# Performance work log

Hardware: AMD Instinct MI355X
Metric: run time of the kernel (lower is better)

## Reference

```python
import jax, jax.numpy as jnp
import numpy as np

N = 50000
E = 800000
F_IN = 96
HID = 128
NCLS = 40
EPS = 0.0  # GINConv default eps


def _mlp(h, W1, b1, W2, b2):
    # Linear -> ReLU -> Linear
    h = jax.nn.relu(h @ W1 + b1)
    return h @ W2 + b2


def _gin_conv(x, edge_index, W1, b1, W2, b2):
    src, dst = edge_index[0], edge_index[1]
    # sum-aggregate neighbor features: scatter-add x[src] into dst
    agg = jax.ops.segment_sum(x[src], dst, num_segments=N)
    return _mlp((1.0 + EPS) * x + agg, W1, b1, W2, b2)


def setup_inputs() -> dict:
    key = jax.random.key(0)
    ks = jax.random.split(key, 12)

    def lin(kw, fan_in, fan_out):
        bound = 1.0 / np.sqrt(fan_in)
        k1, k2 = jax.random.split(kw)
        W = jax.random.uniform(k1, (fan_in, fan_out), jnp.float32, -bound, bound)
        b = jax.random.uniform(k2, (fan_out,), jnp.float32, -bound, bound)
        return W, b

    x = jax.random.normal(ks[0], (N, F_IN), jnp.float32)
    edge_index = jax.random.randint(ks[1], (2, E), 0, N, jnp.int64)
    W1a, b1a = lin(ks[2], F_IN, HID)
    W2a, b2a = lin(ks[3], HID, HID)
    W1b, b1b = lin(ks[4], HID, HID)
    W2b, b2b = lin(ks[5], HID, HID)
    Wfc, bfc = lin(ks[6], HID, NCLS)
    return {"x": x, "edge_index": edge_index,
            "W1a": W1a, "b1a": b1a, "W2a": W2a, "b2a": b2a,
            "W1b": W1b, "b1b": b1b, "W2b": W2b, "b2b": b2b,
            "Wfc": Wfc, "bfc": bfc}


def reference(x, edge_index, W1a, b1a, W2a, b2a, W1b, b1b, W2b, b2b, Wfc, bfc):
    h = _gin_conv(x, edge_index, W1a, b1a, W2a, b2a)
    h = jax.nn.relu(h)
    h = _gin_conv(h, edge_index, W1b, b1b, W2b, b2b)
    return h @ Wfc + bfc  # [N, NCLS]
```

## Files before the change

### kernel.cpp

```cpp
#include <hip/hip_runtime.h>

constexpr int N_NODES = 50000;
constexpr int N_EDGES = 800000;
constexpr int F_INPUT = 96;
constexpr int HID = 128;
constexpr int NCLS = 40;
constexpr int CAP = 64;

typedef __attribute__((ext_vector_type(8))) short short8;
typedef __attribute__((ext_vector_type(4))) float f32x4;

__device__ __forceinline__ float bf2f(unsigned int u16) {
    unsigned int x = u16 << 16;
    return __builtin_bit_cast(float, x);
}
__device__ __forceinline__ unsigned short f2bf(float f) {
    unsigned int x = __builtin_bit_cast(unsigned int, f);
    x += 0x7fffu + ((x >> 16) & 1u);
    return (unsigned short)(x >> 16);
}

__global__ __launch_bounds__(256) void prep_all(
    const float* __restrict__ x,
    const float* __restrict__ W1a, const float* __restrict__ W2a,
    const float* __restrict__ W1b, const float* __restrict__ W2b,
    const float* __restrict__ b2b, const float* __restrict__ Wfc,
    const float* __restrict__ bfc, const int* __restrict__ ei,
    unsigned short* __restrict__ W1aT, unsigned short* __restrict__ W2aT,
    unsigned short* __restrict__ W1bT, unsigned short* __restrict__ WcT,
    float* __restrict__ bc, int* __restrict__ cnt,
    unsigned short* __restrict__ bucket, unsigned short* __restrict__ xb) {
    const int b = blockIdx.x;
    const int tid = threadIdx.x;
    if (b < 33) {
        int idx = b * 256 + tid;
        if (idx < 64 * 128) {
            int n = idx >> 7, k = idx & 127;
            float s = 0.f;
            if (n < NCLS) {
                for (int j = 0; j < 128; ++j) s += W2b[k * 128 + j] * Wfc[j * NCLS + n];
            }
            WcT[idx] = f2bf(s);
        } else if (idx < 64 * 128 + 64) {
            int n = idx - 64 * 128;
            float s = 0.f;
            if (n < NCLS) {
                s = bfc[n];
                for (int j = 0; j < 128; ++j) s += b2b[j] * Wfc[j * NCLS + n];
            }
            bc[n] = s;
        }
    } else if (b < 81) {
        int idx = (b - 33) * 256 + tid;
        int n = idx / 96, k = idx % 96;
        W1aT[idx] = f2bf(W1a[k * 128 + n]);
    } else if (b < 145) {
        int idx = (b - 81) * 256 + tid;
        int n = idx >> 7, k = idx & 127;
        W2aT[idx] = f2bf(W2a[k * 128 + n]);
    } else if (b < 209) {
        int idx = (b - 145) * 256 + tid;
        int n = idx >> 7, k = idx & 127;
        W1bT[idx] = f2bf(W1b[k * 128 + n]);
    } else if (b < 991) {
        int e4 = ((b - 209) * 256 + tid) * 4;
        if (e4 < N_EDGES) {
            int4 s = *reinterpret_cast<const int4*>(&ei[e4]);
            int4 d = *reinterpret_cast<const int4*>(&ei[N_EDGES + e4]);
            int p0 = atomicAdd(&cnt[d.x], 1);
            if (p0 < CAP) bucket[d.x * CAP + p0] = (unsigned short)s.x;
            int p1 = atomicAdd(&cnt[d.y], 1);
            if (p1 < CAP) bucket[d.y * CAP + p1] = (unsigned short)s.y;
            int p2 = atomicAdd(&cnt[d.z], 1);
            if (p2 < CAP) bucket[d.z * CAP + p2] = (unsigned short)s.z;
            int p3 = atomicAdd(&cnt[d.w], 1);
            if (p3 < CAP) bucket[d.w * CAP + p3] = (unsigned short)s.w;
        }
    } else {
        int e4 = ((b - 991) * 256 + tid) * 4;
        if (e4 < N_NODES * F_INPUT) {
            float4 v = *reinterpret_cast<const float4*>(&x[e4]);
            uint2 o;
            o.x = (unsigned int)f2bf(v.x) | ((unsigned int)f2bf(v.y) << 16);
            o.y = (unsigned int)f2bf(v.z) | ((unsigned int)f2bf(v.w) << 16);
            *reinterpret_cast<uint2*>(&xb[e4]) = o;
        }
    }
}

template<int F>
__global__ __launch_bounds__(256) void gather_bf(const unsigned short* __restrict__ X,
                                                 const int* __restrict__ cnt,
                                                 const unsigned short* __restrict__ bucket,
                                                 unsigned short* __restrict__ OUT) {
    const int wave = threadIdx.x >> 6;
    const int lane = threadIdx.x & 63;
    const int node = blockIdx.x * 4 + wave;
    if (node >= N_NODES) return;
    int deg = cnt[node];
    if (deg > CAP) deg = CAP;
    const unsigned short* idx = &bucket[node * CAP];
    const int f = lane * 2;
    const bool act = (f < F);
    float a0 = 0.f, a1 = 0.f;
    int j = 0;
    for (; j + 3 < deg; j += 4) {
        int s0 = idx[j], s1 = idx[j + 1], s2 = idx[j + 2], s3 = idx[j + 3];
        if (act) {
            unsigned int v0 = *reinterpret_cast<const unsigned int*>(&X[(size_t)s0 * F + f]);
            unsigned int v1 = *reinterpret_cast<const unsigned int*>(&X[(size_t)s1 * F + f]);
            unsigned int v2 = *reinterpret_cast<const unsigned int*>(&X[(size_t)s2 * F + f]);
            unsigned int v3 = *reinterpret_cast<const unsigned int*>(&X[(size_t)s3 * F + f]);
            a0 += bf2f(v0 & 0xffff) + bf2f(v1 & 0xffff) + bf2f(v2 & 0xffff) + bf2f(v3 & 0xffff);
            a1 += bf2f(v0 >> 16) + bf2f(v1 >> 16) + bf2f(v2 >> 16) + bf2f(v3 >> 16);
        }
    }
    for (; j < deg; ++j) {
        int s0 = idx[j];
        if (act) {
            unsigned int v = *reinterpret_cast<const unsigned int*>(&X[(size_t)s0 * F + f]);
            a0 += bf2f(v & 0xffff);
            a1 += bf2f(v >> 16);
        }
    }
    if (act) {
        unsigned int xv = *reinterpret_cast<const unsigned int*>(&X[(size_t)node * F + f]);
        a0 += bf2f(xv & 0xffff);
        a1 += bf2f(xv >> 16);
        unsigned int o = (unsigned int)f2bf(a0) | ((unsigned int)f2bf(a1) << 16);
        *reinterpret_cast<unsigned int*>(&OUT[(size_t)node * F + f]) = o;
    }
}

template<int K1, int NT2, int NCOUT, bool RELU2, bool BF16_OUT>
__global__ __launch_bounds__(256) void mlp_fused(const unsigned short* __restrict__ A,
                                                 const unsigned short* __restrict__ W1T,
                                                 const float* __restrict__ b1,
                                                 const unsigned short* __restrict__ W2T,
                                                 const float* __restrict__ b2,
                                                 void* __restrict__ Cout, int M) {
    constexpr int KS1 = K1 / 32;
    constexpr int NT1 = 8;
    constexpr int K2 = 128;
    constexpr int KS2 = K2 / 32;
    __shared__ __align__(16) unsigned short sH[4][16][136];

    const int tid = threadIdx.x;
    const int lane = tid & 63;
    const int wv = tid >> 6;
    const int rowbase = blockIdx.x * 64 + wv * 16;
    const int rA = lane & 15;
    const int kg = lane >> 4;

    int r0 = rowbase + rA;
    if (r0 >= M) r0 = M - 1;
    const unsigned short* ap = A + (size_t)r0 * K1 + kg * 8;
    const unsigned short* b1p = W1T + (size_t)rA * K1 + kg * 8;

    f32x4 acc1[NT1] = {};
#pragma unroll
    for (int ks = 0; ks < KS1; ++ks) {
        short8 a = *reinterpret_cast<const short8*>(ap + ks * 32);
#pragma unroll
        for (int nt = 0; nt < NT1; ++nt) {
            short8 b = *reinterpret_cast<const short8*>(b1p + nt * 16 * K1 + ks * 32);
            acc1[nt] = __builtin_amdgcn_mfma_f32_16x16x32_bf16(a, b, acc1[nt], 0, 0, 0);
        }
    }

    const int oc = lane & 15;
    const int orow = (lane >> 4) * 4;
#pragma unroll
    for (int nt = 0; nt < NT1; ++nt) {
        float bz = b1[nt * 16 + oc];
#pragma unroll
        for (int r = 0; r < 4; ++r) {
            float v = fmaxf(acc1[nt][r] + bz, 0.f);
            sH[wv][orow + r][nt * 16 + oc] = f2bf(v);
        }
    }
    __syncthreads();

    const unsigned short* b2p = W2T + (size_t)rA * K2 + kg * 8;
    f32x4 acc2[NT2] = {};
#pragma unroll
    for (int ks = 0; ks < KS2; ++ks) {
        short8 a = *reinterpret_cast<const short8*>(&sH[wv][rA][kg * 8 + ks * 32]);
#pragma unroll
        for (int nt = 0; nt < NT2; ++nt) {
            short8 b = *reinterpret_cast<const short8*>(b2p + nt * 16 * K2 + ks * 32);
            acc2[nt] = __builtin_amdgcn_mfma_f32_16x16x32_bf16(a, b, acc2[nt], 0, 0, 0);
        }
    }

#pragma unroll
    for (int nt = 0; nt < NT2; ++nt) {
        int col = nt * 16 + oc;
        if (col >= NCOUT) continue;
        float bz = b2[col];
#pragma unroll
        for (int r = 0; r < 4; ++r) {
            int row = rowbase + orow + r;
            if (row < M) {
                float v = acc2[nt][r] + bz;
                if (RELU2) v = fmaxf(v, 0.f);
                if (BF16_OUT)
                    ((unsigned short*)Cout)[(size_t)row * NCOUT + col] = f2bf(v);
                else
                    ((float*)Cout)[(size_t)row * NCOUT + col] = v;
            }
        }
    }
}

extern "C" void kernel_launch(void* const* d_in, const int* in_sizes, int n_in,
                              void* d_out, int out_size, void* d_ws, size_t ws_size,
                              hipStream_t stream) {
    const float* x   = (const float*)d_in[0];
    const int*   ei  = (const int*)d_in[1];
    const float* W1a = (const float*)d_in[2];
    const float* b1a = (const float*)d_in[3];
    const float* W2a = (const float*)d_in[4];
    const float* b2a = (const float*)d_in[5];
    const float* W1b = (const float*)d_in[6];
    const float* b1b = (const float*)d_in[7];
    const float* W2b = (const float*)d_in[8];
    const float* b2b = (const float*)d_in[9];
    const float* Wfc = (const float*)d_in[10];
    const float* bfc = (const float*)d_in[11];
    float* out = (float*)d_out;

    char* p = (char*)d_ws;
    auto alloc = [&](size_t bytes) {
        char* r = p;
        p += (bytes + 255) & ~size_t(255);
        return r;
    };
    unsigned short* xb   = (unsigned short*)alloc((size_t)N_NODES * F_INPUT * 2);
    unsigned short* h0   = (unsigned short*)alloc((size_t)N_NODES * F_INPUT * 2);
    unsigned short* t    = (unsigned short*)alloc((size_t)N_NODES * HID * 2);
    unsigned short* g    = (unsigned short*)alloc((size_t)N_NODES * HID * 2);
    unsigned short* W1aT = (unsigned short*)alloc(128 * 96 * 2);
    unsigned short* W2aT = (unsigned short*)alloc(128 * 128 * 2);
    unsigned short* W1bT = (unsigned short*)alloc(128 * 128 * 2);
    unsigned short* WcT  = (unsigned short*)alloc(64 * 128 * 2);
    float* bc            = (float*)alloc(64 * 4);
    int* cnt             = (int*)alloc(N_NODES * 4);
    unsigned short* bucket = (unsigned short*)alloc((size_t)N_NODES * CAP * 2);

    const int xb4 = (N_NODES * F_INPUT / 4 + 255) / 256;
    const int nb4 = (N_NODES + 3) / 4;
    const int mb = (N_NODES + 63) / 64;

    hipMemsetAsync(cnt, 0, N_NODES * sizeof(int), stream);

    prep_all<<<991 + xb4, 256, 0, stream>>>(x, W1a, W2a, W1b, W2b, b2b, Wfc, bfc, ei,
                                            W1aT, W2aT, W1bT, WcT, bc, cnt, bucket, xb);

    gather_bf<F_INPUT><<<nb4, 256, 0, stream>>>(xb, cnt, bucket, h0);
    mlp_fused<96, 8, 128, true, true><<<mb, 256, 0, stream>>>(h0, W1aT, b1a, W2aT, b2a, t,
                                                              N_NODES);

    gather_bf<HID><<<nb4, 256, 0, stream>>>(t, cnt, bucket, g);
    mlp_fused<128, 4, 40, false, false><<<mb, 256, 0, stream>>>(g, W1bT, b1b, WcT, bc, out,
                                                                N_NODES);
}
```

Baseline: 269.7 us.

## Sort neighbor lists per wave and broadcast indices via shuffles in gather

The gather kernel now loads each node's bucket of neighbor indices into lanes once and bitonic-sorts them with warp shuffles. The goal is deterministic, ascending-address access, which should also give better cache locality. Indices are broadcast with __shfl instead of being re-read from memory, and the main loop is unrolled to 8 loads in flight. The prep kernel is reordered so the edge-bucketing blocks run first with one edge per thread instead of four, and the weight prep blocks run last. The sort adds about 21 shuffle steps per node, which may cost more than the reuse it buys.

```diff
diff --git a/kernel.cpp b/kernel.cpp
--- a/kernel.cpp
+++ b/kernel.cpp
@@ -19,6 +19,15 @@
     x += 0x7fffu + ((x >> 16) & 1u);
     return (unsigned short)(x >> 16);
 }
+
+constexpr int PB_FILL = N_EDGES / 256;
+constexpr int PB_XC = (N_NODES * F_INPUT / 4 + 255) / 256;
+constexpr int PB_X0 = PB_FILL;
+constexpr int PB_F0 = PB_X0 + PB_XC;
+constexpr int PB_W1 = PB_F0 + 33;
+constexpr int PB_W2 = PB_W1 + 48;
+constexpr int PB_W3 = PB_W2 + 64;
+constexpr int PB_END = PB_W3 + 64;
 
 __global__ __launch_bounds__(256) void prep_all(
     const float* __restrict__ x,
@@ -32,8 +41,23 @@
     unsigned short* __restrict__ bucket, unsigned short* __restrict__ xb) {
     const int b = blockIdx.x;
     const int tid = threadIdx.x;
-    if (b < 33) {
-        int idx = b * 256 + tid;
+    if (b < PB_FILL) {
+        int e = b * 256 + tid;
+        int s = ei[e];
+        int d = ei[N_EDGES + e];
+        int pos = atomicAdd(&cnt[d], 1);
+        if (pos < CAP) bucket[d * CAP + pos] = (unsigned short)s;
+    } else if (b < PB_F0) {
+        int e4 = ((b - PB_X0) * 256 + tid) * 4;
+        if (e4 < N_NODES * F_INPUT) {
+            float4 v = *reinterpret_cast<const float4*>(&x[e4]);
+            uint2 o;
+            o.x = (unsigned int)f2bf(v.x) | ((unsigned int)f2bf(v.y) << 16);
+            o.y = (unsigned int)f2bf(v.z) | ((unsigned int)f2bf(v.w) << 16);
+            *reinterpret_cast<uint2*>(&xb[e4]) = o;
+        }
+    } else if (b < PB_W1) {
+        int idx = (b - PB_F0) * 256 + tid;
         if (idx < 64 * 128) {
             int n = idx >> 7, k = idx & 127;
             float s = 0.f;
@@ -50,41 +74,18 @@
             }
             bc[n] = s;
         }
-    } else if (b < 81) {
-        int idx = (b - 33) * 256 + tid;
+    } else if (b < PB_W2) {
+        int idx = (b - PB_W1) * 256 + tid;
         int n = idx / 96, k = idx % 96;
         W1aT[idx] = f2bf(W1a[k * 128 + n]);
-    } else if (b < 145) {
-        int idx = (b - 81) * 256 + tid;
+    } else if (b < PB_W3) {
+        int idx = (b - PB_W2) * 256 + tid;
         int n = idx >> 7, k = idx & 127;
         W2aT[idx] = f2bf(W2a[k * 128 + n]);
-    } else if (b < 209) {
-        int idx = (b - 145) * 256 + tid;
+    } else {
+        int idx = (b - PB_W3) * 256 + tid;
         int n = idx >> 7, k = idx & 127;
         W1bT[idx] = f2bf(W1b[k * 128 + n]);
-    } else if (b < 991) {
-        int e4 = ((b - 209) * 256 + tid) * 4;
-        if (e4 < N_EDGES) {
-            int4 s = *reinterpret_cast<const int4*>(&ei[e4]);
-            int4 d = *reinterpret_cast<const int4*>(&ei[N_EDGES + e4]);
-            int p0 = atomicAdd(&cnt[d.x], 1);
-            if (p0 < CAP) bucket[d.x * CAP + p0] = (unsigned short)s.x;
-            int p1 = atomicAdd(&cnt[d.y], 1);
-            if (p1 < CAP) bucket[d.y * CAP + p1] = (unsigned short)s.y;
-            int p2 = atomicAdd(&cnt[d.z], 1);
-            if (p2 < CAP) bucket[d.z * CAP + p2] = (unsigned short)s.z;
-            int p3 = atomicAdd(&cnt[d.w], 1);
-            if (p3 < CAP) bucket[d.w * CAP + p3] = (unsigned short)s.w;
-        }
-    } else {
-        int e4 = ((b - 991) * 256 + tid) * 4;
-        if (e4 < N_NODES * F_INPUT) {
-            float4 v = *reinterpret_cast<const float4*>(&x[e4]);
-            uint2 o;
-            o.x = (unsigned int)f2bf(v.x) | ((unsigned int)f2bf(v.y) << 16);
-            o.y = (unsigned int)f2bf(v.z) | ((unsigned int)f2bf(v.w) << 16);
-            *reinterpret_cast<uint2*>(&xb[e4]) = o;
-        }
     }
 }
 
@@ -99,28 +100,63 @@
     if (node >= N_NODES) return;
     int deg = cnt[node];
     if (deg > CAP) deg = CAP;
-    const unsigned short* idx = &bucket[node * CAP];
+
+    int v = (lane < deg) ? (int)bucket[node * CAP + lane] : 0x7fffffff;
+#pragma unroll
+    for (int k = 2; k <= 64; k <<= 1) {
+#pragma unroll
+        for (int j = k >> 1; j > 0; j >>= 1) {
+            int pv = __shfl_xor(v, j, 64);
+            bool keepmin = (((lane & k) == 0) == ((lane & j) == 0));
+            v = keepmin ? (pv < v ? pv : v) : (pv > v ? pv : v);
+        }
+    }
+
     const int f = lane * 2;
     const bool act = (f < F);
     float a0 = 0.f, a1 = 0.f;
     int j = 0;
-    for (; j + 3 < deg; j += 4) {
-        int s0 = idx[j], s1 = idx[j + 1], s2 = idx[j + 2], s3 = idx[j + 3];
+    for (; j + 7 < deg; j += 8) {
+        int s[8];
+        unsigned int vv[8];
+#pragma unroll
+        for (int q = 0; q < 8; ++q) s[q] = __shfl(v, j + q, 64);
+#pragma unroll
+        for (int q = 0; q < 8; ++q) {
+            if (act) vv[q] = *reinterpret_cast<const unsigned int*>(&X[(size_t)s[q] * F + f]);
+        }
         if (act) {
-            unsigned int v0 = *reinterpret_cast<const unsigned int*>(&X[(size_t)s0 * F + f]);
-            unsigned int v1 = *reinterpret_cast<const unsigned int*>(&X[(size_t)s1 * F + f]);
-            unsigned int v2 = *reinterpret_cast<const unsigned int*>(&X[(size_t)s2 * F + f]);
-            unsigned int v3 = *reinterpret_cast<const unsigned int*>(&X[(size_t)s3 * F + f]);
-            a0 += bf2f(v0 & 0xffff) + bf2f(v1 & 0xffff) + bf2f(v2 & 0xffff) + bf2f(v3 & 0xffff);
-            a1 += bf2f(v0 >> 16) + bf2f(v1 >> 16) + bf2f(v2 >> 16) + bf2f(v3 >> 16);
-        }
+#pragma unroll
+            for (int q = 0; q < 8; ++q) {
+                a0 += bf2f(vv[q] & 0xffff);
+                a1 += bf2f(vv[q] >> 16);
+            }
+        }
+    }
+    if (j + 3 < deg) {
+        int s[4];
+        unsigned int vv[4];
+#pragma unroll
+        for (int q = 0; q < 4; ++q) s[q] = __shfl(v, j + q, 64);
+#pragma unroll
+        for (int q = 0; q < 4; ++q) {
+            if (act) vv[q] = *reinterpret_cast<const unsigned int*>(&X[(size_t)s[q] * F + f]);
+        }
+        if (act) {
+#pragma unroll
+            for (int q = 0; q < 4; ++q) {
+                a0 += bf2f(vv[q] & 0xffff);
+                a1 += bf2f(vv[q] >> 16);
+            }
+        }
+        j += 4;
     }
     for (; j < deg; ++j) {
-        int s0 = idx[j];
+        int s = __shfl(v, j, 64);
         if (act) {
-            unsigned int v = *reinterpret_cast<const unsigned int*>(&X[(size_t)s0 * F + f]);
-            a0 += bf2f(v & 0xffff);
-            a1 += bf2f(v >> 16);
+            unsigned int vx = *reinterpret_cast<const unsigned int*>(&X[(size_t)s * F + f]);
+            a0 += bf2f(vx & 0xffff);
+            a1 += bf2f(vx >> 16);
         }
     }
     if (act) {
@@ -248,14 +284,13 @@
     int* cnt             = (int*)alloc(N_NODES * 4);
     unsigned short* bucket = (unsigned short*)alloc((size_t)N_NODES * CAP * 2);
 
-    const int xb4 = (N_NODES * F_INPUT / 4 + 255) / 256;
     const int nb4 = (N_NODES + 3) / 4;
     const int mb = (N_NODES + 63) / 64;
 
     hipMemsetAsync(cnt, 0, N_NODES * sizeof(int), stream);
 
-    prep_all<<<991 + xb4, 256, 0, stream>>>(x, W1a, W2a, W1b, W2b, b2b, Wfc, bfc, ei,
-                                            W1aT, W2aT, W1bT, WcT, bc, cnt, bucket, xb);
+    prep_all<<<PB_END, 256, 0, stream>>>(x, W1a, W2a, W1b, W2b, b2b, Wfc, bfc, ei,
+                                         W1aT, W2aT, W1bT, WcT, bc, cnt, bucket, xb);
 
     gather_bf<F_INPUT><<<nb4, 256, 0, stream>>>(xb, cnt, bucket, h0);
     mlp_fused<96, 8, 128, true, true><<<mb, 256, 0, stream>>>(h0, W1aT, b1a, W2aT, b2a, t,
```

After: 260.3 us. -3.5%, faster.
